# Performance work log

Measured on AMD Instinct MI355X. Metric: run time of the kernel, lower is better.

The kernel has to match this reference:

```python
import jax, jax.numpy as jnp
import numpy as np

B, D, H, DM, O = 8192, 512, 1024, 2048, 256


def setup_inputs() -> dict:
    key = jax.random.key(0)
    ks = jax.random.split(key, 24)
    def rn(k, shape, scale=1.0):
        return jax.random.normal(k, shape, dtype=jnp.float32) * scale
    w = 0.02  # weight init scale
    return {
        "x":  rn(ks[0], (B, D)),
        "h0": rn(ks[1], (B, H), 0.1), "h1": rn(ks[2], (B, H), 0.1),
        "c0": rn(ks[3], (B, H), 0.1), "c1": rn(ks[4], (B, H), 0.1),
        # Bernoulli keep masks with model_prob=1.0 -> all ones
        "m0": jnp.ones((B, H), jnp.float32), "m1": jnp.ones((B, H), jnp.float32),
        # layer 0 gate weights: in = D + H = 1536
        "Wf0": rn(ks[5], (D + H, H), w), "bf0": jnp.full((H,), 0.01, jnp.float32),
        "Wi0": rn(ks[6], (D + H, H), w), "bi0": jnp.full((H,), 0.01, jnp.float32),
        "Wc0": rn(ks[7], (D + H, H), w), "bc0": jnp.full((H,), 0.01, jnp.float32),
        "Wo0": rn(ks[8], (D + H, H), w), "bo0": jnp.full((H,), 0.01, jnp.float32),
        # layer 1 gate weights: in = H + H = 2048
        "Wf1": rn(ks[9],  (2 * H, H), w), "bf1": jnp.full((H,), 0.01, jnp.float32),
        "Wi1": rn(ks[10], (2 * H, H), w), "bi1": jnp.full((H,), 0.01, jnp.float32),
        "Wc1": rn(ks[11], (2 * H, H), w), "bc1": jnp.full((H,), 0.01, jnp.float32),
        "Wo1": rn(ks[12], (2 * H, H), w), "bo1": jnp.full((H,), 0.01, jnp.float32),
        # output MLP: H -> DM -> O (identity activation per default nn.Sequential())
        "Wm1": rn(ks[13], (H, DM), w), "bm1": jnp.full((DM,), 0.01, jnp.float32),
        "Wm2": rn(ks[14], (DM, O), w), "bm2": jnp.full((O,), 0.01, jnp.float32),
    }


def _lstm_cell(comb, c, Wf, bf, Wi, bi, Wc, bc, Wo, bo):
    # fuse the 4 gate GEMMs into one matmul, then split
    W = jnp.concatenate([Wf, Wi, Wc, Wo], axis=1)      # [in, 4H]
    b = jnp.concatenate([bf, bi, bc, bo])               # [4H]
    g = comb @ W + b                                    # [B, 4H]
    f, i, ct, o = jnp.split(g, 4, axis=1)
    c_new = jax.nn.sigmoid(f) * c + jax.nn.sigmoid(i) * jnp.tanh(ct)
    h_new = jax.nn.sigmoid(o) * jnp.tanh(c_new)
    return h_new, c_new


def reference(x, h0, h1, c0, c1, m0, m1,
              Wf0, bf0, Wi0, bi0, Wc0, bc0, Wo0, bo0,
              Wf1, bf1, Wi1, bi1, Wc1, bc1, Wo1, bo1,
              Wm1, bm1, Wm2, bm2):
    # layer 0: combined = cat(input, h0 * mask0)
    comb0 = jnp.concatenate([x, h0 * m0], axis=1)       # [B, D+H]
    h0n, c0n = _lstm_cell(comb0, c0, Wf0, bf0, Wi0, bi0, Wc0, bc0, Wo0, bo0)
    # layer 1: combined = cat(h0_new * mask0, h1 * mask1)
    comb1 = jnp.concatenate([h0n * m0, h1 * m1], axis=1)  # [B, 2H]
    h1n, c1n = _lstm_cell(comb1, c1, Wf1, bf1, Wi1, bi1, Wc1, bc1, Wo1, bo1)
    # output MLP (dropout p=0 is identity; activation is identity Sequential)
    out = (h1n @ Wm1 + bm1) @ Wm2 + bm2                 # [B, O]
    return out, h0n, h1n, c0n, c1n
```

## Files before the change

kernel.cpp:

```cpp
#include <hip/hip_runtime.h>
#include <hip/hip_bf16.h>
#include <cstdint>
#include <cstddef>

#define DI __device__ __forceinline__

typedef __attribute__((ext_vector_type(8))) short short8;
typedef __attribute__((ext_vector_type(4))) float f32x4;

static constexpr int Bb = 8192, Dd = 512, Hh = 1024;

DI short f2b(float f) {
  union { __hip_bfloat16 h; short s; } u;
  u.h = __float2bfloat16(f);
  return u.s;
}

DI float sigm(float x) {
  float e = __builtin_amdgcn_exp2f(-1.4426950408889634f * x);
  return __builtin_amdgcn_rcpf(1.0f + e);
}
DI float tanh_(float x) {
  float xc = fminf(fmaxf(x, -20.0f), 20.0f);
  float e = __builtin_amdgcn_exp2f(-2.8853900817779268f * xc);
  return (1.0f - e) * __builtin_amdgcn_rcpf(1.0f + e);
}

DI void gload16(const void* g, void* l) {
  __builtin_amdgcn_global_load_lds(
      (const __attribute__((address_space(1))) uint32_t*)g,
      (__attribute__((address_space(3))) uint32_t*)l, 16, 0, 0);
}


__global__ void conv_acts(const float* __restrict__ x, const float* __restrict__ h0,
                          const float* __restrict__ m0, const float* __restrict__ h1,
                          const float* __restrict__ m1,
                          short* __restrict__ A0, short* __restrict__ A1) {
  const int row = blockIdx.x, t = threadIdx.x;
  float v[8];
  if (t < 192) {
    if (t < 64) {
      const float4* p = (const float4*)(x + (size_t)row * Dd + t * 8);
      float4 a = p[0], b = p[1];
      v[0] = a.x; v[1] = a.y; v[2] = a.z; v[3] = a.w;
      v[4] = b.x; v[5] = b.y; v[6] = b.z; v[7] = b.w;
    } else {
      const int j = t * 8 - 512;
      const float4* ph = (const float4*)(h0 + (size_t)row * Hh + j);
      const float4* pm = (const float4*)(m0 + (size_t)row * Hh + j);
      float4 a = ph[0], b = ph[1], ma = pm[0], mb = pm[1];
      v[0] = a.x * ma.x; v[1] = a.y * ma.y; v[2] = a.z * ma.z; v[3] = a.w * ma.w;
      v[4] = b.x * mb.x; v[5] = b.y * mb.y; v[6] = b.z * mb.z; v[7] = b.w * mb.w;
    }
    short8 o;
    #pragma unroll
    for (int q = 0; q < 8; q++) o[q] = f2b(v[q]);
    *(short8*)(A0 + (size_t)row * 1536 + t * 8) = o;
  } else {
    const int j = (t - 192) * 8;
    const float4* ph = (const float4*)(h1 + (size_t)row * Hh + j);
    const float4* pm = (const float4*)(m1 + (size_t)row * Hh + j);
    float4 a = ph[0], b = ph[1], ma = pm[0], mb = pm[1];
    v[0] = a.x * ma.x; v[1] = a.y * ma.y; v[2] = a.z * ma.z; v[3] = a.w * ma.w;
    v[4] = b.x * mb.x; v[5] = b.y * mb.y; v[6] = b.z * mb.z; v[7] = b.w * mb.w;
    short8 o;
    #pragma unroll
    for (int q = 0; q < 8; q++) o[q] = f2b(v[q]);
    *(short8*)(A1 + (size_t)row * 2048 + 1024 + j) = o;
  }
}

__global__ void transpose_all(
    const float* __restrict__ w00, const float* __restrict__ w01,
    const float* __restrict__ w02, const float* __restrict__ w03,
    const float* __restrict__ w10, const float* __restrict__ w11,
    const float* __restrict__ w12, const float* __restrict__ w13,
    short* __restrict__ WT0, short* __restrict__ WT1) {
  __shared__ float t[64][65];
  const int z = blockIdx.z;
  const int layer = z >> 2, g = z & 3;
  const int K = layer ? 2048 : 1536;
  const int k0 = blockIdx.x * 64;
  if (k0 >= K) return;
  const float* src;
  switch (z) {
    case 0: src = w00; break; case 1: src = w01; break;
    case 2: src = w02; break; case 3: src = w03; break;
    case 4: src = w10; break; case 5: src = w11; break;
    case 6: src = w12; break; default: src = w13; break;
  }
  short* dst = layer ? WT1 : WT0;
  const int n0 = blockIdx.y * 64;
  const int tid = threadIdx.x;
  const int r = tid >> 2, c0 = (tid & 3) * 16;
  const float* s = src + (size_t)(k0 + r) * 1024 + n0 + c0;
  #pragma unroll
  for (int q = 0; q < 16; q += 4) {
    float4 v = *(const float4*)(s + q);
    t[r][c0 + q + 0] = v.x; t[r][c0 + q + 1] = v.y;
    t[r][c0 + q + 2] = v.z; t[r][c0 + q + 3] = v.w;
  }
  __syncthreads();
  const int n = n0 + r;
  const int j = (n >> 4) * 64 + g * 16 + (n & 15);
  short8 o0, o1;
  #pragma unroll
  for (int q = 0; q < 8; q++) o0[q] = f2b(t[c0 + q][r]);
  #pragma unroll
  for (int q = 0; q < 8; q++) o1[q] = f2b(t[c0 + 8 + q][r]);
  short* d = dst + (size_t)j * K + k0 + c0;
  *(short8*)d = o0;
  *((short8*)d + 1) = o1;
}

__global__ void mlp_prep(const float* __restrict__ Wm1, short* __restrict__ Wm1b,
                         const float* __restrict__ Wm2, short* __restrict__ Wm2T,
                         const float* __restrict__ bm1, const float* __restrict__ bm2,
                         float* __restrict__ bp) {
  __shared__ float t[64][65];
  const int b = blockIdx.x, tid = threadIdx.x;
  if (b < 1024) {
    const int id = b * 256 + tid;
    const float4* p = (const float4*)(Wm1 + (size_t)id * 8);
    float4 a = p[0], bb = p[1];
    short8 o;
    o[0] = f2b(a.x); o[1] = f2b(a.y); o[2] = f2b(a.z); o[3] = f2b(a.w);
    o[4] = f2b(bb.x); o[5] = f2b(bb.y); o[6] = f2b(bb.z); o[7] = f2b(bb.w);
    *(short8*)(Wm1b + (size_t)id * 8) = o;
  } else if (b < 1152) {
    const int b2 = b - 1024;
    const int k0 = (b2 & 31) * 64, n0 = (b2 >> 5) * 64;
    const int r = tid >> 2, c0 = (tid & 3) * 16;
    const float* s = Wm2 + (size_t)(k0 + r) * 256 + n0 + c0;
    #pragma unroll
    for (int q = 0; q < 16; q += 4) {
      float4 v = *(const float4*)(s + q);
      t[r][c0 + q + 0] = v.x; t[r][c0 + q + 1] = v.y;
      t[r][c0 + q + 2] = v.z; t[r][c0 + q + 3] = v.w;
    }
    __syncthreads();
    const int n = n0 + r;
    short8 o0, o1;
    #pragma unroll
    for (int q = 0; q < 8; q++) o0[q] = f2b(t[c0 + q][r]);
    #pragma unroll
    for (int q = 0; q < 8; q++) o1[q] = f2b(t[c0 + 8 + q][r]);
    short* d = Wm2T + (size_t)n * 2048 + k0 + c0;
    *(short8*)d = o0;
    *((short8*)d + 1) = o1;
  } else {
    __shared__ float red[16][17];
    const int o0 = (b - 1152) * 16;
    const int oo = tid & 15, kk = tid >> 4;
    float s = 0.f;
    const int kbase = kk * 128;
    #pragma unroll 4
    for (int k = 0; k < 128; k++)
      s += bm1[kbase + k] * Wm2[(size_t)(kbase + k) * 256 + o0 + oo];
    red[kk][oo] = s;
    __syncthreads();
    if (tid < 16) {
      float acc = bm2[o0 + tid];
      #pragma unroll
      for (int j = 0; j < 16; j++) acc += red[j][tid];
      bp[o0 + tid] = acc;
    }
  }
}

__global__ __launch_bounds__(256) void gemm_bt0(
    const short* __restrict__ A, const short* __restrict__ Bt, int K,
    short* __restrict__ Cb, int ldc) {
  __shared__ __align__(16) short sA[128 * 32];
  __shared__ __align__(16) short sB[128 * 32];
  const int tid = threadIdx.x;
  const int lane = tid & 63;
  const int wave = tid >> 6;
  const int wm = wave >> 1, wn = wave & 1;
  const int bm = blockIdx.x, bn = blockIdx.y;
  const int lr = lane & 15, lq = lane >> 4;

  f32x4 acc[4][4] = {};

  const short* pA = A + ((size_t)(bm * 128 + (tid >> 2))) * K + (tid & 3) * 8;
  const short* pB = Bt + ((size_t)(bn * 128 + (tid >> 2))) * K + (tid & 3) * 8;
  short* lA = sA + tid * 8;
  short* lB = sB + tid * 8;
  const int aoff = (wm * 64 + lr) * 32 + lq * 8;
  const int boff = (wn * 64 + lr) * 32 + lq * 8;

  for (int k0 = 0; k0 < K; k0 += 32) {
    gload16(pA + k0, lA);
    gload16(pA + (size_t)64 * K + k0, lA + 2048);
    gload16(pB + k0, lB);
    gload16(pB + (size_t)64 * K + k0, lB + 2048);
    __syncthreads();
    short8 af[4], bv[4];
    #pragma unroll
    for (int m = 0; m < 4; m++) af[m] = *(const short8*)&sA[aoff + m * 512];
    #pragma unroll
    for (int n = 0; n < 4; n++) bv[n] = *(const short8*)&sB[boff + n * 512];
    #pragma unroll
    for (int m = 0; m < 4; m++)
      #pragma unroll
      for (int n = 0; n < 4; n++)
        acc[m][n] = __builtin_amdgcn_mfma_f32_16x16x32_bf16(af[m], bv[n], acc[m][n], 0, 0, 0);
    __syncthreads();
  }

  const int crow0 = bm * 128 + wm * 64 + lq * 4;
  const int ccol0 = bn * 128 + wn * 64 + lr;
  #pragma unroll
  for (int m = 0; m < 4; m++)
    #pragma unroll
    for (int r = 0; r < 4; r++) {
      const int row = crow0 + m * 16 + r;
      #pragma unroll
      for (int n = 0; n < 4; n++)
        Cb[(size_t)row * ldc + ccol0 + n * 16] = f2b(acc[m][n][r]);
    }
}

__global__ __launch_bounds__(256) void gemm_out(
    const short* __restrict__ A, const short* __restrict__ Bt, int K,
    float* __restrict__ outp, const float* __restrict__ bpv) {
  __shared__ __align__(16) short sA[64 * 32];
  __shared__ __align__(16) short sB[128 * 32];
  const int tid = threadIdx.x;
  const int lane = tid & 63;
  const int wn = tid >> 6;
  const int bm = blockIdx.x, bn = blockIdx.y;
  const int lr = lane & 15, lq = lane >> 4;

  f32x4 acc[4][2] = {};

  const short* pA = A + ((size_t)(bm * 64 + (tid >> 2))) * K + (tid & 3) * 8;
  const short* pB = Bt + ((size_t)(bn * 128 + (tid >> 2))) * K + (tid & 3) * 8;
  short* lA = sA + tid * 8;
  short* lB = sB + tid * 8;
  const int boff = (wn * 32 + lr) * 32 + lq * 8;

  for (int k0 = 0; k0 < K; k0 += 32) {
    gload16(pA + k0, lA);
    gload16(pB + k0, lB);
    gload16(pB + (size_t)64 * K + k0, lB + 2048);
    __syncthreads();
    short8 af[4], bv[2];
    #pragma unroll
    for (int m = 0; m < 4; m++) af[m] = *(const short8*)&sA[(m * 16 + lr) * 32 + lq * 8];
    #pragma unroll
    for (int n = 0; n < 2; n++) bv[n] = *(const short8*)&sB[boff + n * 512];
    #pragma unroll
    for (int m = 0; m < 4; m++)
      #pragma unroll
      for (int n = 0; n < 2; n++)
        acc[m][n] = __builtin_amdgcn_mfma_f32_16x16x32_bf16(af[m], bv[n], acc[m][n], 0, 0, 0);
    __syncthreads();
  }

  const int crow0 = bm * 64 + lq * 4;
  const int ccol0 = bn * 128 + wn * 32 + lr;
  float bvv[2];
  #pragma unroll
  for (int n = 0; n < 2; n++) bvv[n] = bpv[ccol0 + n * 16];
  #pragma unroll
  for (int m = 0; m < 4; m++)
    #pragma unroll
    for (int r = 0; r < 4; r++) {
      const int row = crow0 + m * 16 + r;
      #pragma unroll
      for (int n = 0; n < 2; n++)
        outp[(size_t)row * 256 + ccol0 + n * 16] = acc[m][n][r] + bvv[n];
    }
}


#define STA(buf, h, kt) { const short* s_ = gA + (size_t)(h) * 64 * K + (size_t)(kt) * 64; \
    gload16(s_ + aS0, &sA[buf][h][tid * 8]);                                               \
    gload16(s_ + aS1, &sA[buf][h][4096 + tid * 8]); }
#define STB(buf, h, kt) { const short* s_ = gB + (size_t)(h) * 128 * K + (size_t)(kt) * 64; \
    gload16(s_ + bS0, &sB[buf][h][tid * 8]);                                                \
    gload16(s_ + bS1, &sB[buf][h][4096 + tid * 8]); }

#define LDB(buf) {                                                \
    const short* bb = &sB[buf][bh][brb];                          \
    _Pragma("unroll") for (int n = 0; n < 4; n++) {               \
      bv[n][0] = *(const short8*)(bb + n * 1024 + sw0);           \
      bv[n][1] = *(const short8*)(bb + n * 1024 + sw1); } }

#define LDA_(buf, q, av) {                                        \
    const short* ab = &sA[buf][(q) >> 1][arb + ((q) & 1) * 2048]; \
    av[0][0] = *(const short8*)(ab + sw0);                        \
    av[0][1] = *(const short8*)(ab + sw1);                        \
    av[1][0] = *(const short8*)(ab + 1024 + sw0);                 \
    av[1][1] = *(const short8*)(ab + 1024 + sw1); }

#define MM(q, av) {                                               \
    __builtin_amdgcn_s_setprio(1);                                \
    _Pragma("unroll") for (int m = 0; m < 2; m++)                 \
    _Pragma("unroll") for (int n = 0; n < 4; n++) {               \
      acc[2*(q)+m][n] = __builtin_amdgcn_mfma_f32_16x16x32_bf16(av[m][0], bv[n][0], acc[2*(q)+m][n], 0, 0, 0); \
      acc[2*(q)+m][n] = __builtin_amdgcn_mfma_f32_16x16x32_bf16(av[m][1], bv[n][1], acc[2*(q)+m][n], 0, 0, 0); } \
    __builtin_amdgcn_s_setprio(0); }

#define BARR() __builtin_amdgcn_s_barrier()
#define VM6()  asm volatile("s_waitcnt vmcnt(6)")
#define LG8()  asm volatile("s_waitcnt lgkmcnt(8)")
#define LG0()  asm volatile("s_waitcnt lgkmcnt(0)")

#define PH(buf, q, STG, vm) { short8 av[2][2]; LDA_(buf, q, av); STG; \
    if (vm) VM6(); BARR(); LG0(); MM(q, av); BARR(); }

__global__ __launch_bounds__(512, 2) void gemm8_lstm(
    const short* __restrict__ A, const short* __restrict__ Bt, const int K,
    const float* __restrict__ cprev, float* __restrict__ hout,
    float* __restrict__ cout, short* __restrict__ anext, const int ldan,
    const float* __restrict__ mask,
    const float* __restrict__ bF, const float* __restrict__ bI,
    const float* __restrict__ bC, const float* __restrict__ bO) {
  __shared__ __align__(16) short sA[2][2][8192];
  __shared__ __align__(16) short sB[2][2][8192];
  const int tid = threadIdx.x;
  const int lane = tid & 63, wid = tid >> 6;
  const int wr = wid >> 2, wc = wid & 3;
  const int lr = lane & 15, lq = lane >> 4;
  const int bm = blockIdx.x, bn = blockIdx.y;

  const int NT = K >> 6;
  const int NIT = NT >> 1;

  const int r0 = tid >> 3;
  const int csw = (tid & 7) ^ (r0 & 7);
  const int growA0 = ((r0 >> 5) & 1) * 32 + (r0 & 31);
  const int growA1 = 128 + growA0;
  const size_t aS0 = (size_t)growA0 * K + csw * 8;
  const size_t aS1 = (size_t)growA1 * K + csw * 8;
  const size_t bS0 = (size_t)r0 * K + csw * 8;
  const size_t bS1 = (size_t)(r0 + 64) * K + csw * 8;
  const short* gA = A + (size_t)bm * 256 * K;
  const short* gB = Bt + (size_t)bn * 256 * K;

  const int arb = (wr * 64 + lr) * 64;
  const int brb = ((wc & 1) * 64 + lr) * 64;
  const int bh = wc >> 1;
  const int sw0 = ((lq) ^ (lr & 7)) * 8;
  const int sw1 = ((4 + lq) ^ (lr & 7)) * 8;

  f32x4 acc[8][4] = {};
  short8 bv[4][2];

  STB(0, 0, 0); STB(0, 1, 0); STA(0, 0, 0); STA(0, 1, 0);
  STB(1, 0, 1); STB(1, 1, 1); STA(1, 0, 1);
  VM6(); BARR();

  for (int it = 0; it < NIT; ++it) {
    const int k1 = 2 * it + 1;
    int t2 = 2 * it + 2; if (t2 >= NT) t2 = 0;
    int t3 = 2 * it + 3; if (t3 >= NT) t3 = 1;
    { short8 av[2][2]; LDB(0); LDA_(0, 0, av); STA(1, 1, k1);
      LG8(); BARR(); LG0(); MM(0, av); BARR(); }
    PH(0, 1, STB(0, 0, t2), 0);
    PH(0, 2, STB(0, 1, t2), 0);
    PH(0, 3, STA(0, 0, t2), 1);
    { short8 av[2][2]; LDB(1); LDA_(1, 0, av); STA(0, 1, t2);
      LG8(); BARR(); LG0(); MM(0, av); BARR(); }
    PH(1, 1, STB(1, 0, t3), 0);
    PH(1, 2, STB(1, 1, t3), 0);
    PH(1, 3, STA(1, 0, t3), 1);
  }

  const int n = (bn * 4 + wc) * 16 + lr;
  const float bf_ = bF[n], bi_ = bI[n], bc_ = bC[n], bo_ = bO[n];
  const int row0 = bm * 256 + wr * 128 + lq * 4;

  float cp[4], mk[4], cpn[4], mkn[4];
  #pragma unroll
  for (int rr = 0; rr < 4; rr++) {
    const size_t idx = (size_t)(row0 + rr) * 1024 + n;
    cp[rr] = cprev[idx];
    mk[rr] = mask ? mask[idx] : 1.0f;
  }
  #pragma unroll
  for (int mf = 0; mf < 8; mf++) {
    if (mf < 7) {
      #pragma unroll
      for (int rr = 0; rr < 4; rr++) {
        const size_t idx2 = (size_t)(row0 + (mf + 1) * 16 + rr) * 1024 + n;
        cpn[rr] = cprev[idx2];
        mkn[rr] = mask ? mask[idx2] : 1.0f;
      }
    }
    #pragma unroll
    for (int rr = 0; rr < 4; rr++) {
      const int row = row0 + mf * 16 + rr;
      const size_t idx = (size_t)row * 1024 + n;
      const float fg = sigm(acc[mf][0][rr] + bf_);
      const float ig = sigm(acc[mf][1][rr] + bi_);
      const float cg = tanh_(acc[mf][2][rr] + bc_);
      const float og = sigm(acc[mf][3][rr] + bo_);
      const float cn = fg * cp[rr] + ig * cg;
      const float hn = og * tanh_(cn);
      cout[idx] = cn;
      hout[idx] = hn;
      anext[(size_t)row * ldan + n] = f2b(hn * mk[rr]);
    }
    #pragma unroll
    for (int rr = 0; rr < 4; rr++) { cp[rr] = cpn[rr]; mk[rr] = mkn[rr]; }
  }
}


extern "C" void kernel_launch(void* const* d_in, const int* in_sizes, int n_in,
                              void* d_out, int out_size, void* d_ws, size_t ws_size,
                              hipStream_t stream) {
  (void)in_sizes; (void)n_in; (void)out_size; (void)ws_size;
  const float* x   = (const float*)d_in[0];
  const float* h0  = (const float*)d_in[1];
  const float* h1  = (const float*)d_in[2];
  const float* c0  = (const float*)d_in[3];
  const float* c1  = (const float*)d_in[4];
  const float* m0  = (const float*)d_in[5];
  const float* m1  = (const float*)d_in[6];
  const float* Wf0 = (const float*)d_in[7];  const float* bf0 = (const float*)d_in[8];
  const float* Wi0 = (const float*)d_in[9];  const float* bi0 = (const float*)d_in[10];
  const float* Wc0 = (const float*)d_in[11]; const float* bc0 = (const float*)d_in[12];
  const float* Wo0 = (const float*)d_in[13]; const float* bo0 = (const float*)d_in[14];
  const float* Wf1 = (const float*)d_in[15]; const float* bf1 = (const float*)d_in[16];
  const float* Wi1 = (const float*)d_in[17]; const float* bi1 = (const float*)d_in[18];
  const float* Wc1 = (const float*)d_in[19]; const float* bc1 = (const float*)d_in[20];
  const float* Wo1 = (const float*)d_in[21]; const float* bo1 = (const float*)d_in[22];
  const float* Wm1 = (const float*)d_in[23]; const float* bm1 = (const float*)d_in[24];
  const float* Wm2 = (const float*)d_in[25]; const float* bm2 = (const float*)d_in[26];

  float* dout  = (float*)d_out;
  float* out_o = dout;
  float* h0n   = dout + 2097152;
  float* h1n   = h0n + 8388608;
  float* c0n   = h1n + 8388608;
  float* c1n   = c0n + 8388608;

  char* ws = (char*)d_ws;
  short* A0   = (short*)(ws);
  short* A1   = (short*)(ws + 25165824);
  short* A2   = (short*)(ws + 58720256);
  short* WT0  = (short*)(ws + 75497472);
  short* WT1  = (short*)(ws + 88080384);
  short* Wm1b = (short*)(ws + 104857600);
  short* Wm2T = (short*)(ws + 109051904);
  short* WpT  = (short*)(ws + 110100480);
  float* bp   = (float*)(ws + 110624768);

  conv_acts<<<dim3(8192), dim3(320), 0, stream>>>(x, h0, m0, h1, m1, A0, A1);
  transpose_all<<<dim3(32, 16, 8), dim3(256), 0, stream>>>(
      Wf0, Wi0, Wc0, Wo0, Wf1, Wi1, Wc1, Wo1, WT0, WT1);
  mlp_prep<<<dim3(1168), dim3(256), 0, stream>>>(Wm1, Wm1b, Wm2, Wm2T, bm1, bm2, bp);

  gemm_bt0<<<dim3(2, 8), dim3(256), 0, stream>>>(Wm2T, Wm1b, 2048, WpT, 1024);

  gemm8_lstm<<<dim3(32, 16), dim3(512), 0, stream>>>(
      A0, WT0, 1536, c0, h0n, c0n, A1, 2048, m0, bf0, bi0, bc0, bo0);

  gemm8_lstm<<<dim3(32, 16), dim3(512), 0, stream>>>(
      A1, WT1, 2048, c1, h1n, c1n, A2, 1024, nullptr, bf1, bi1, bc1, bo1);

  gemm_out<<<dim3(128, 2), dim3(256), 0, stream>>>(A2, WpT, 1024, out_o, bp);
}
```

Measured before the change: 391.7 us.

## Software-pipeline LDS fragment reads one phase ahead with double-buffered registers

Restructures the GEMM main loop so the A and B fragment loads from LDS for the next MFMA phase are issued before the current phase's MFMAs. Ping-pong register buffers (avA/avB, bv0/bv1) replace the per-phase wait-for-all-LDS, and the waits become partial lgkmcnt counts. The global-to-LDS stage order and vmcnt thresholds are reshuffled to fit. This is meant to hide LDS latency behind matrix math, at the cost of more VGPRs and fragile hand-counted waitcnt values.

```diff
diff --git a/kernel.cpp b/kernel.cpp
--- a/kernel.cpp
+++ b/kernel.cpp
@@ -283,11 +283,11 @@
     gload16(s_ + bS0, &sB[buf][h][tid * 8]);                                                \
     gload16(s_ + bS1, &sB[buf][h][4096 + tid * 8]); }
 
-#define LDB(buf) {                                                \
+#define LDB(buf, bvx) {                                           \
     const short* bb = &sB[buf][bh][brb];                          \
     _Pragma("unroll") for (int n = 0; n < 4; n++) {               \
-      bv[n][0] = *(const short8*)(bb + n * 1024 + sw0);           \
-      bv[n][1] = *(const short8*)(bb + n * 1024 + sw1); } }
+      bvx[n][0] = *(const short8*)(bb + n * 1024 + sw0);          \
+      bvx[n][1] = *(const short8*)(bb + n * 1024 + sw1); } }
 
 #define LDA_(buf, q, av) {                                        \
     const short* ab = &sA[buf][(q) >> 1][arb + ((q) & 1) * 2048]; \
@@ -296,21 +296,19 @@
     av[1][0] = *(const short8*)(ab + 1024 + sw0);                 \
     av[1][1] = *(const short8*)(ab + 1024 + sw1); }
 
-#define MM(q, av) {                                               \
+#define MM(q, av, bvx) {                                          \
     __builtin_amdgcn_s_setprio(1);                                \
     _Pragma("unroll") for (int m = 0; m < 2; m++)                 \
     _Pragma("unroll") for (int n = 0; n < 4; n++) {               \
-      acc[2*(q)+m][n] = __builtin_amdgcn_mfma_f32_16x16x32_bf16(av[m][0], bv[n][0], acc[2*(q)+m][n], 0, 0, 0); \
-      acc[2*(q)+m][n] = __builtin_amdgcn_mfma_f32_16x16x32_bf16(av[m][1], bv[n][1], acc[2*(q)+m][n], 0, 0, 0); } \
+      acc[2*(q)+m][n] = __builtin_amdgcn_mfma_f32_16x16x32_bf16(av[m][0], bvx[n][0], acc[2*(q)+m][n], 0, 0, 0); \
+      acc[2*(q)+m][n] = __builtin_amdgcn_mfma_f32_16x16x32_bf16(av[m][1], bvx[n][1], acc[2*(q)+m][n], 0, 0, 0); } \
     __builtin_amdgcn_s_setprio(0); }
 
-#define BARR() __builtin_amdgcn_s_barrier()
-#define VM6()  asm volatile("s_waitcnt vmcnt(6)")
-#define LG8()  asm volatile("s_waitcnt lgkmcnt(8)")
-#define LG0()  asm volatile("s_waitcnt lgkmcnt(0)")
-
-#define PH(buf, q, STG, vm) { short8 av[2][2]; LDA_(buf, q, av); STG; \
-    if (vm) VM6(); BARR(); LG0(); MM(q, av); BARR(); }
+#define BARR()  __builtin_amdgcn_s_barrier()
+#define VM6()   asm volatile("s_waitcnt vmcnt(6)")
+#define VM4()   asm volatile("s_waitcnt vmcnt(4)")
+#define LGK4()  asm volatile("s_waitcnt lgkmcnt(4)")
+#define LGK12() asm volatile("s_waitcnt lgkmcnt(12)")
 
 __global__ __launch_bounds__(512, 2) void gemm8_lstm(
     const short* __restrict__ A, const short* __restrict__ Bt, const int K,
@@ -348,26 +346,26 @@
   const int sw1 = ((4 + lq) ^ (lr & 7)) * 8;
 
   f32x4 acc[8][4] = {};
-  short8 bv[4][2];
+  short8 bv0[4][2], bv1[4][2];
+  short8 avA[2][2], avB[2][2];
 
   STB(0, 0, 0); STB(0, 1, 0); STA(0, 0, 0); STA(0, 1, 0);
   STB(1, 0, 1); STB(1, 1, 1); STA(1, 0, 1);
   VM6(); BARR();
+  LDB(0, bv0); LDA_(0, 0, avA);
 
   for (int it = 0; it < NIT; ++it) {
     const int k1 = 2 * it + 1;
     int t2 = 2 * it + 2; if (t2 >= NT) t2 = 0;
     int t3 = 2 * it + 3; if (t3 >= NT) t3 = 1;
-    { short8 av[2][2]; LDB(0); LDA_(0, 0, av); STA(1, 1, k1);
-      LG8(); BARR(); LG0(); MM(0, av); BARR(); }
-    PH(0, 1, STB(0, 0, t2), 0);
-    PH(0, 2, STB(0, 1, t2), 0);
-    PH(0, 3, STA(0, 0, t2), 1);
-    { short8 av[2][2]; LDB(1); LDA_(1, 0, av); STA(0, 1, t2);
-      LG8(); BARR(); LG0(); MM(0, av); BARR(); }
-    PH(1, 1, STB(1, 0, t3), 0);
-    PH(1, 2, STB(1, 1, t3), 0);
-    PH(1, 3, STA(1, 0, t3), 1);
+    LDA_(0, 1, avB); STA(1, 1, k1); BARR(); LGK4(); MM(0, avA, bv0); BARR();
+    LDA_(0, 2, avA); STB(0, 0, t2); BARR(); LGK4(); MM(1, avB, bv0); BARR();
+    LDA_(0, 3, avB); STB(0, 1, t2); VM4(); BARR(); LGK4(); MM(2, avA, bv0); BARR();
+    LDB(1, bv1); LDA_(1, 0, avA); STA(0, 0, t2); BARR(); LGK12(); MM(3, avB, bv0); BARR();
+    LDA_(1, 1, avB); STA(0, 1, t2); BARR(); LGK4(); MM(0, avA, bv1); BARR();
+    LDA_(1, 2, avA); STB(1, 0, t3); BARR(); LGK4(); MM(1, avB, bv1); BARR();
+    LDA_(1, 3, avB); STB(1, 1, t3); VM4(); BARR(); LGK4(); MM(2, avA, bv1); BARR();
+    LDB(0, bv0); LDA_(0, 0, avA); STA(1, 0, t3); BARR(); LGK12(); MM(3, avB, bv1); BARR();
   }
 
   const int n = (bn * 4 + wc) * 16 + lr;
```

Measured after the change: 409.8 us. 4.6% more time.
